# Kernel tuning notes

Hardware: AMD Instinct MI355X
Metric: run time of the kernel (lower is better)

## Reference

```python
import jax, jax.numpy as jnp
import numpy as np
from jax import lax

AR_ORDER = 8
SEQ_LEN = 4096
BATCH = 8192
REGRESSOR_DIM = AR_ORDER + 1  # ar_order past outputs + 1 (zeroed) exogenous term


def setup_inputs() -> dict:
    key = jax.random.key(0)
    k1, k2, k3 = jax.random.split(key, 3)
    y = jax.random.normal(k1, (BATCH, AR_ORDER), dtype=jnp.float32)
    u = jax.random.normal(k2, (BATCH, SEQ_LEN), dtype=jnp.float32)
    # scale weights so the linear recurrence is stable over 4096 steps
    W = jax.random.normal(k3, (1, REGRESSOR_DIM), dtype=jnp.float32) * 0.05
    return {"y": y, "u": u, "W": W}


def reference(y, u, W):
    # Faithful ARX forward: output[:, :ar] = y, then for each t,
    ar = y.shape[1]
    seq = u.shape[1]
    w_ar = W[0, :ar]          # coefficients on past outputs
    # W[0, ar] multiplies the zeroed exogenous term -> contributes 0

    def step(carry, _):
        # carry: [B, ar] = last ar outputs (oldest first)
        pred = carry @ w_ar                                   # [B]
        new_carry = jnp.concatenate([carry[:, 1:], pred[:, None]], axis=1)
        return new_carry, pred

    _, preds = lax.scan(step, y, xs=None, length=seq)         # preds: [seq, B]
    return jnp.concatenate([y, preds.T], axis=1)              # [B, seq + ar]
```

## Files before the change

### kernel.cpp

```cpp
#include <hip/hip_runtime.h>

#define AR 8
#define SEQ 4096
#define BATCH 8192
#define OUTW (AR + SEQ)

typedef float f32x4 __attribute__((ext_vector_type(4)));

__global__ __launch_bounds__(256, 4) void arx_fused_kernel(const float* __restrict__ y,
                                                           const float* __restrict__ W,
                                                           float* __restrict__ out) {
    __shared__ float P[12][AR][AR];
    __shared__ float w[AR];
    const int tid = threadIdx.x;

    if (tid < AR) w[tid] = W[tid];
    __syncthreads();

    if (tid < 64) {
        const int i = tid >> 3, j = tid & 7;
        P[0][i][j] = (i == 7) ? w[j] : ((i == j - 1) ? 1.f : 0.f);
    }
    __syncthreads();

    for (int k = 0; k < 11; ++k) {
        if (tid < 64) {
            const int i = tid >> 3, j = tid & 7;
            float v = 0.f;
            #pragma unroll
            for (int q = 0; q < AR; ++q) v += P[k][i][q] * P[k][q][j];
            P[k + 1][i][j] = v;
        }
        __syncthreads();
    }

    const int tt = blockIdx.x * 256 + tid;
    const int t0 = tt * 4;

    float c[4][AR];
    {
        float r[AR];
        #pragma unroll
        for (int j = 0; j < AR; ++j) r[j] = w[j];
        #pragma unroll
        for (int k = 2; k < 12; ++k) {
            if ((t0 >> k) & 1) {
                float nr[AR];
                #pragma unroll
                for (int j = 0; j < AR; ++j) {
                    float s = 0.f;
                    #pragma unroll
                    for (int q = 0; q < AR; ++q) s += r[q] * P[k][q][j];
                    nr[j] = s;
                }
                #pragma unroll
                for (int j = 0; j < AR; ++j) r[j] = nr[j];
            }
        }
        #pragma unroll
        for (int j = 0; j < AR; ++j) c[0][j] = r[j];
        #pragma unroll
        for (int k = 1; k < 4; ++k) {
            const float c7 = c[k - 1][AR - 1];
            c[k][0] = c7 * w[0];
            #pragma unroll
            for (int j = 1; j < AR; ++j) c[k][j] = c[k - 1][j - 1] + c7 * w[j];
        }
    }

    for (int rg = blockIdx.y; rg < BATCH / 8; rg += gridDim.y) {
        const int row0 = rg * 8;

        float yy[8][AR];
        #pragma unroll
        for (int r = 0; r < 8; ++r) {
            const f32x4* yv = reinterpret_cast<const f32x4*>(y + (size_t)(row0 + r) * AR);
            f32x4 a = yv[0], b = yv[1];
            yy[r][0] = a.x; yy[r][1] = a.y; yy[r][2] = a.z; yy[r][3] = a.w;
            yy[r][4] = b.x; yy[r][5] = b.y; yy[r][6] = b.z; yy[r][7] = b.w;
        }

        #pragma unroll
        for (int r = 0; r < 8; ++r) {
            float s[4];
            #pragma unroll
            for (int k = 0; k < 4; ++k) {
                float acc = 0.f;
                #pragma unroll
                for (int j = 0; j < AR; ++j) acc += c[k][j] * yy[r][j];
                s[k] = acc;
            }
            *reinterpret_cast<f32x4*>(out + (size_t)(row0 + r) * OUTW + AR + t0) =
                (f32x4){s[0], s[1], s[2], s[3]};
        }

        if (blockIdx.x == 0 && threadIdx.x < 16) {
            const int r = threadIdx.x >> 1, part = threadIdx.x & 1;
            const int row = row0 + r;
            reinterpret_cast<f32x4*>(out + (size_t)row * OUTW)[part] =
                reinterpret_cast<const f32x4*>(y + (size_t)row * AR)[part];
        }
    }
}

extern "C" void kernel_launch(void* const* d_in, const int* in_sizes, int n_in,
                              void* d_out, int out_size, void* d_ws, size_t ws_size,
                              hipStream_t stream) {
    const float* y = (const float*)d_in[0];
    const float* W = (const float*)d_in[2];
    float* out = (float*)d_out;

    arx_fused_kernel<<<dim3(SEQ / 1024, 256), 256, 0, stream>>>(y, W, out);
}
```

Measured before the change: 27.44 us.

## Assign whole rows per block with 16 coefficient sets per thread

Each block now covers a full output row per iteration: every thread holds 16 time-step coefficient vectors and writes 4 float4 chunks strided by 256. The extra coefficients are built from the first 4 using the P^1024 and P^2048 powers. This cuts the setup work of building c per thread and gives each row one y load instead of per-column-tile loads. In exchange the register footprint rises (launch bounds drop to 2 blocks per CU), which may reduce occupancy for this store-bound kernel.

```diff
diff --git a/kernel.cpp b/kernel.cpp
--- a/kernel.cpp
+++ b/kernel.cpp
@@ -4,10 +4,11 @@
 #define SEQ 4096
 #define BATCH 8192
 #define OUTW (AR + SEQ)
+#define NB 1024
 
 typedef float f32x4 __attribute__((ext_vector_type(4)));
 
-__global__ __launch_bounds__(256, 4) void arx_fused_kernel(const float* __restrict__ y,
+__global__ __launch_bounds__(256, 2) void arx_fused_kernel(const float* __restrict__ y,
                                                            const float* __restrict__ W,
                                                            float* __restrict__ out) {
     __shared__ float P[12][AR][AR];
@@ -34,16 +35,14 @@
         __syncthreads();
     }
 
-    const int tt = blockIdx.x * 256 + tid;
-    const int t0 = tt * 4;
-
-    float c[4][AR];
+    float c[16][AR];
     {
+        const int t0 = tid * 4;
         float r[AR];
         #pragma unroll
         for (int j = 0; j < AR; ++j) r[j] = w[j];
         #pragma unroll
-        for (int k = 2; k < 12; ++k) {
+        for (int k = 2; k < 10; ++k) {
             if ((t0 >> k) & 1) {
                 float nr[AR];
                 #pragma unroll
@@ -66,39 +65,59 @@
             #pragma unroll
             for (int j = 1; j < AR; ++j) c[k][j] = c[k - 1][j - 1] + c7 * w[j];
         }
+        #pragma unroll
+        for (int k = 0; k < 4; ++k) {
+            #pragma unroll
+            for (int j = 0; j < AR; ++j) {
+                float s = 0.f;
+                #pragma unroll
+                for (int q = 0; q < AR; ++q) s += c[k][q] * P[10][q][j];
+                c[4 + k][j] = s;
+            }
+        }
+        #pragma unroll
+        for (int k = 0; k < 4; ++k) {
+            #pragma unroll
+            for (int j = 0; j < AR; ++j) {
+                float s = 0.f;
+                #pragma unroll
+                for (int q = 0; q < AR; ++q) s += c[k][q] * P[11][q][j];
+                c[8 + k][j] = s;
+            }
+        }
+        #pragma unroll
+        for (int k = 0; k < 4; ++k) {
+            #pragma unroll
+            for (int j = 0; j < AR; ++j) {
+                float s = 0.f;
+                #pragma unroll
+                for (int q = 0; q < AR; ++q) s += c[4 + k][q] * P[11][q][j];
+                c[12 + k][j] = s;
+            }
+        }
     }
 
-    for (int rg = blockIdx.y; rg < BATCH / 8; rg += gridDim.y) {
-        const int row0 = rg * 8;
+    for (int row = blockIdx.x; row < BATCH; row += NB) {
+        const f32x4* yv = reinterpret_cast<const f32x4*>(y + (size_t)row * AR);
+        const f32x4 a = yv[0], b = yv[1];
+        const float yy[AR] = {a.x, a.y, a.z, a.w, b.x, b.y, b.z, b.w};
 
-        float yy[8][AR];
+        float* rowp = out + (size_t)row * OUTW;
+
+        if (tid < 2) reinterpret_cast<f32x4*>(rowp)[tid] = (tid == 0) ? a : b;
+
+        f32x4* pred = reinterpret_cast<f32x4*>(rowp + AR);
         #pragma unroll
-        for (int r = 0; r < 8; ++r) {
-            const f32x4* yv = reinterpret_cast<const f32x4*>(y + (size_t)(row0 + r) * AR);
-            f32x4 a = yv[0], b = yv[1];
-            yy[r][0] = a.x; yy[r][1] = a.y; yy[r][2] = a.z; yy[r][3] = a.w;
-            yy[r][4] = b.x; yy[r][5] = b.y; yy[r][6] = b.z; yy[r][7] = b.w;
-        }
-
-        #pragma unroll
-        for (int r = 0; r < 8; ++r) {
-            float s[4];
+        for (int s = 0; s < 4; ++s) {
+            float v[4];
             #pragma unroll
             for (int k = 0; k < 4; ++k) {
                 float acc = 0.f;
                 #pragma unroll
-                for (int j = 0; j < AR; ++j) acc += c[k][j] * yy[r][j];
-                s[k] = acc;
+                for (int j = 0; j < AR; ++j) acc += c[4 * s + k][j] * yy[j];
+                v[k] = acc;
             }
-            *reinterpret_cast<f32x4*>(out + (size_t)(row0 + r) * OUTW + AR + t0) =
-                (f32x4){s[0], s[1], s[2], s[3]};
-        }
-
-        if (blockIdx.x == 0 && threadIdx.x < 16) {
-            const int r = threadIdx.x >> 1, part = threadIdx.x & 1;
-            const int row = row0 + r;
-            reinterpret_cast<f32x4*>(out + (size_t)row * OUTW)[part] =
-                reinterpret_cast<const f32x4*>(y + (size_t)row * AR)[part];
+            pred[tid + 256 * s] = (f32x4){v[0], v[1], v[2], v[3]};
         }
     }
 }
@@ -110,5 +129,5 @@
     const float* W = (const float*)d_in[2];
     float* out = (float*)d_out;
 
-    arx_fused_kernel<<<dim3(SEQ / 1024, 256), 256, 0, stream>>>(y, W, out);
+    arx_fused_kernel<<<NB, 256, 0, stream>>>(y, W, out);
 }
```

Measured after the change: 32.63 us. +18.9%, slower.
